# Kernel tuning notes

Measured on AMD Instinct MI355X. Metric: run time of the kernel, lower is better.

The kernel has to match this reference:

```python
import jax, jax.numpy as jnp
import numpy as np

NB, NSITES, N_NGB, DIM, NG = 32, 65536, 13, 3, 48


def setup_inputs() -> dict:
    key = jax.random.key(0)
    k1, k2, k3, k4, k5 = jax.random.split(key, 5)
    In = jax.random.normal(k1, (NB, 1, NSITES), dtype=jnp.float32)
    # wtVC ~ Normal(mean=1.0, std=0.1), size (dim, N_ngb)
    wtVC = 1.0 + 0.1 * jax.random.normal(k2, (DIM, N_NGB), dtype=jnp.float32)
    # gdiags: (Ng*dim, Ng*dim) symmetry-rotation mixing matrix
    gdiags = jax.random.normal(k3, (NG * DIM, NG * DIM), dtype=jnp.float32)
    GnnPerms = jax.random.randint(k4, (NG, N_NGB), 0, N_NGB)
    NNsites = jax.random.randint(k5, (N_NGB, NSITES), 0, NSITES)
    return {"In": In, "wtVC": wtVC, "gdiags": gdiags,
            "GnnPerms": GnnPerms, "NNsites": NNsites}


def reference(In, wtVC, gdiags, GnnPerms, NNsites):
    Ng = GnnPerms.shape[0]
    dim, n_ngb = wtVC.shape
    # RotateParams: row g*dim+d of the permuted weight is wtVC[d, GnnPerms[g]]
    Wp = wtVC[:, GnnPerms]                              # [dim, Ng, N_ngb]
    Wp = jnp.transpose(Wp, (1, 0, 2)).reshape(Ng * dim, n_ngb)
    Wt = gdiags @ Wp                                    # [Ng*dim, N_ngb]
    # Final op in torch is sum over g / Ng; fold that into the weight to
    # avoid materializing the [Nb, Ng*dim, Nsites] intermediate.
    Wmean = Wt.reshape(Ng, dim, n_ngb).mean(axis=0)     # [dim, N_ngb]
    # RearrangeInput: gathered[b, j, s] = In[b, 0, NNsites[j, s]]
    gathered = In[:, 0, :][:, NNsites]                  # [Nb, N_ngb, Nsites]
    # out[b, d, s] = sum_j Wmean[d, j] * gathered[b, j, s]
    return jnp.einsum('dj,bjs->bds', Wmean, gathered)   # [Nb, dim, Nsites]
```

## Files before the change

### kernel.cpp

```cpp
#include <hip/hip_runtime.h>

#define NB_     32
#define NSITES_ 65536
#define NNGB_   13
#define DIM_    3
#define NG_     48
#define GD_     (NG_ * DIM_)

typedef unsigned uvec4_t __attribute__((ext_vector_type(4)));

__global__ __launch_bounds__(256) void prep_kernel_78486(
    const float* __restrict__ In,
    const float* __restrict__ wtVC,
    const float* __restrict__ gdiags,
    const int*   __restrict__ perms,
    float*  __restrict__ wm,
    ushort* __restrict__ InT,
    int nTransBlocks)
{
    const int t = threadIdx.x;
    if ((int)blockIdx.x < DIM_ * NNGB_) {
        const int p = blockIdx.x;
        const int d = p / NNGB_, j = p - NNGB_ * d;
        __shared__ float wpj[GD_];
        __shared__ float red[4];
        if (t < GD_) {
            int g = t / DIM_, dp = t - DIM_ * g;
            wpj[t] = wtVC[dp * NNGB_ + perms[g * NNGB_ + j]];
        }
        __syncthreads();
        float acc = 0.f;
        for (int e = t; e < NG_ * GD_; e += 256) {
            int g = e / GD_;
            int k = e - g * GD_;
            acc += gdiags[(g * DIM_ + d) * GD_ + k] * wpj[k];
        }
#pragma unroll
        for (int off = 32; off > 0; off >>= 1) acc += __shfl_down(acc, off, 64);
        if ((t & 63) == 0) red[t >> 6] = acc;
        __syncthreads();
        if (t == 0) wm[p] = (red[0] + red[1] + red[2] + red[3]) * (1.0f / NG_);
    } else {
        const int tb = blockIdx.x - DIM_ * NNGB_;
        if (tb >= nTransBlocks) return;
        const int s0 = tb * 64;
        __shared__ ushort tile[64][40];
        const int sl = t & 63, bq = t >> 6;
#pragma unroll
        for (int r = 0; r < 8; r++) {
            int b = bq * 8 + r;
            float v = In[b * NSITES_ + s0 + sl];
            unsigned fu = __float_as_uint(v);
            fu = fu + 0x7FFFu + ((fu >> 16) & 1u);
            tile[sl][b] = (ushort)(fu >> 16);
        }
        __syncthreads();
        const int site = t >> 2, q = t & 3;
        uvec4_t val = *(const uvec4_t*)&tile[site][q * 8];
        *(uvec4_t*)(InT + (size_t)(s0 + site) * NB_ + q * 8) = val;
    }
}

__global__ __launch_bounds__(256) void gather_kernel_78486(
    const ushort* __restrict__ InT,
    const int*    __restrict__ nn,
    const float*  __restrict__ wm,
    float* __restrict__ out)
{
    const int t = blockIdx.x * 256 + threadIdx.x;
    const int q = t & 3;
    const int s = t >> 2;

    int idx[NNGB_];
#pragma unroll
    for (int j = 0; j < NNGB_; j++) idx[j] = nn[j * NSITES_ + s];

    uvec4_t u[NNGB_];
#pragma unroll
    for (int j = 0; j < NNGB_; j++)
        u[j] = *(const uvec4_t*)(InT + ((size_t)idx[j] << 5) + (q << 3));

    float a0[8], a1[8], a2[8];
#pragma unroll
    for (int i = 0; i < 8; i++) { a0[i] = 0.f; a1[i] = 0.f; a2[i] = 0.f; }

#pragma unroll
    for (int j = 0; j < NNGB_; j++) {
        unsigned uu[4] = {u[j].x, u[j].y, u[j].z, u[j].w};
        float v[8];
#pragma unroll
        for (int k = 0; k < 4; k++) {
            v[2 * k]     = __uint_as_float(uu[k] << 16);
            v[2 * k + 1] = __uint_as_float(uu[k] & 0xFFFF0000u);
        }
        float w0 = wm[j], w1 = wm[NNGB_ + j], w2 = wm[2 * NNGB_ + j];
#pragma unroll
        for (int i = 0; i < 8; i++) {
            a0[i] += w0 * v[i];
            a1[i] += w1 * v[i];
            a2[i] += w2 * v[i];
        }
    }

#pragma unroll
    for (int i = 0; i < 8; i++) {
        int b = q * 8 + i;
        size_t base = (size_t)b * DIM_ * NSITES_ + s;
        out[base]               = a0[i];
        out[base + NSITES_]     = a1[i];
        out[base + 2 * NSITES_] = a2[i];
    }
}

__global__ __launch_bounds__(256) void gather_fallback_78486(
    const float* __restrict__ In,
    const int*   __restrict__ nn,
    const float* __restrict__ wm,
    float* __restrict__ out)
{
    const int t = blockIdx.x * 256 + threadIdx.x;
    const int s = t & (NSITES_ - 1);
    const int b = t >> 16;
    float x0 = 0.f, x1 = 0.f, x2 = 0.f;
#pragma unroll
    for (int j = 0; j < NNGB_; j++) {
        int idx = nn[j * NSITES_ + s];
        float v = In[b * NSITES_ + idx];
        x0 += wm[0 * NNGB_ + j] * v;
        x1 += wm[1 * NNGB_ + j] * v;
        x2 += wm[2 * NNGB_ + j] * v;
    }
    out[(b * DIM_ + 0) * NSITES_ + s] = x0;
    out[(b * DIM_ + 1) * NSITES_ + s] = x1;
    out[(b * DIM_ + 2) * NSITES_ + s] = x2;
}

extern "C" void kernel_launch(void* const* d_in, const int* in_sizes, int n_in,
                              void* d_out, int out_size, void* d_ws, size_t ws_size,
                              hipStream_t stream)
{
    const float* In     = (const float*)d_in[0];
    const float* wtVC   = (const float*)d_in[1];
    const float* gdiags = (const float*)d_in[2];
    const int*   perms  = (const int*)d_in[3];
    const int*   nn     = (const int*)d_in[4];
    float* out = (float*)d_out;

    float*  wm  = (float*)d_ws;
    ushort* InT = (ushort*)((char*)d_ws + 1024);

    const size_t need = 1024 + (size_t)NSITES_ * NB_ * sizeof(ushort);
    const int nTrans = NSITES_ / 64;

    if (ws_size >= need) {
        prep_kernel_78486<<<DIM_ * NNGB_ + nTrans, 256, 0, stream>>>(
            In, wtVC, gdiags, perms, wm, InT, nTrans);
        gather_kernel_78486<<<(NSITES_ * 4) / 256, 256, 0, stream>>>(
            InT, nn, wm, out);
    } else {
        prep_kernel_78486<<<DIM_ * NNGB_, 256, 0, stream>>>(
            In, wtVC, gdiags, perms, wm, (ushort*)nullptr, 0);
        gather_fallback_78486<<<(NSITES_ * NB_) / 256, 256, 0, stream>>>(
            In, nn, wm, out);
    }
}
```

Baseline: 93.66 us.

## Fuse prep and gather kernels using a software grid barrier

Merges the weight-prep/transpose kernel and the gather kernel into one persistent-style launch of 1024 blocks. Each block transposes its tile and, for the first 39 blocks, computes the mean weights, then all blocks wait on a global atomic counter before doing the gather. This removes one kernel launch and the gap between kernels, but adds a memset launch and a spin barrier. The barrier relies on all 1024 blocks being co-resident (launch bounds request 4 blocks per SIMD-group), and it would deadlock if they are not.

```diff
diff --git a/kernel.cpp b/kernel.cpp
--- a/kernel.cpp
+++ b/kernel.cpp
@@ -9,23 +9,46 @@
 
 typedef unsigned uvec4_t __attribute__((ext_vector_type(4)));
 
-__global__ __launch_bounds__(256) void prep_kernel_78486(
+__global__ __launch_bounds__(256, 4) void fused_kernel_78486(
     const float* __restrict__ In,
     const float* __restrict__ wtVC,
     const float* __restrict__ gdiags,
     const int*   __restrict__ perms,
-    float*  __restrict__ wm,
-    ushort* __restrict__ InT,
-    int nTransBlocks)
-{
-    const int t = threadIdx.x;
-    if ((int)blockIdx.x < DIM_ * NNGB_) {
-        const int p = blockIdx.x;
+    const int*   __restrict__ nn,
+    float*    __restrict__ wm,
+    ushort*   __restrict__ InT,
+    unsigned* __restrict__ ctr,
+    float*    __restrict__ out)
+{
+    const int t   = threadIdx.x;
+    const int blk = blockIdx.x;
+
+    {
+        const int s0 = blk * 64;
+        __shared__ ushort tile[64][40];
+        const int sl = t & 63, bq = t >> 6;
+#pragma unroll
+        for (int r = 0; r < 8; r++) {
+            int b = bq * 8 + r;
+            float v = In[b * NSITES_ + s0 + sl];
+            unsigned fu = __float_as_uint(v);
+            fu = fu + 0x7FFFu + ((fu >> 16) & 1u);
+            tile[sl][b] = (ushort)(fu >> 16);
+        }
+        __syncthreads();
+        const int site = t >> 2, qq = t & 3;
+        uvec4_t val = *(const uvec4_t*)&tile[site][qq * 8];
+        *(uvec4_t*)(InT + (size_t)(s0 + site) * NB_ + qq * 8) = val;
+    }
+
+    if (blk < DIM_ * NNGB_) {
+        const int p = blk;
         const int d = p / NNGB_, j = p - NNGB_ * d;
         __shared__ float wpj[GD_];
         __shared__ float red[4];
         if (t < GD_) {
-            int g = t / DIM_, dp = t - DIM_ * g;
+            int g = t / DIM_;
+            int dp = t - DIM_ * g;
             wpj[t] = wtVC[dp * NNGB_ + perms[g * NNGB_ + j]];
         }
         __syncthreads();
@@ -40,36 +63,22 @@
         if ((t & 63) == 0) red[t >> 6] = acc;
         __syncthreads();
         if (t == 0) wm[p] = (red[0] + red[1] + red[2] + red[3]) * (1.0f / NG_);
-    } else {
-        const int tb = blockIdx.x - DIM_ * NNGB_;
-        if (tb >= nTransBlocks) return;
-        const int s0 = tb * 64;
-        __shared__ ushort tile[64][40];
-        const int sl = t & 63, bq = t >> 6;
-#pragma unroll
-        for (int r = 0; r < 8; r++) {
-            int b = bq * 8 + r;
-            float v = In[b * NSITES_ + s0 + sl];
-            unsigned fu = __float_as_uint(v);
-            fu = fu + 0x7FFFu + ((fu >> 16) & 1u);
-            tile[sl][b] = (ushort)(fu >> 16);
-        }
-        __syncthreads();
-        const int site = t >> 2, q = t & 3;
-        uvec4_t val = *(const uvec4_t*)&tile[site][q * 8];
-        *(uvec4_t*)(InT + (size_t)(s0 + site) * NB_ + q * 8) = val;
-    }
-}
-
-__global__ __launch_bounds__(256) void gather_kernel_78486(
-    const ushort* __restrict__ InT,
-    const int*    __restrict__ nn,
-    const float*  __restrict__ wm,
-    float* __restrict__ out)
-{
-    const int t = blockIdx.x * 256 + threadIdx.x;
-    const int q = t & 3;
-    const int s = t >> 2;
+    }
+
+    __syncthreads();
+    if (t == 0) {
+        __threadfence();
+        atomicAdd(ctr, 1u);
+        while (__hip_atomic_load(ctr, __ATOMIC_RELAXED,
+                                 __HIP_MEMORY_SCOPE_AGENT) < 1024u)
+            __builtin_amdgcn_s_sleep(8);
+        __threadfence();
+    }
+    __syncthreads();
+
+    const int gt = blk * 256 + t;
+    const int q  = gt & 3;
+    const int s  = gt >> 2;
 
     int idx[NNGB_];
 #pragma unroll
@@ -112,6 +121,35 @@
     }
 }
 
+__global__ __launch_bounds__(256) void prep_kernel_78486(
+    const float* __restrict__ wtVC,
+    const float* __restrict__ gdiags,
+    const int*   __restrict__ perms,
+    float*  __restrict__ wm)
+{
+    const int t = threadIdx.x;
+    const int p = blockIdx.x;
+    const int d = p / NNGB_, j = p - NNGB_ * d;
+    __shared__ float wpj[GD_];
+    __shared__ float red[4];
+    if (t < GD_) {
+        int g = t / DIM_, dp = t - DIM_ * g;
+        wpj[t] = wtVC[dp * NNGB_ + perms[g * NNGB_ + j]];
+    }
+    __syncthreads();
+    float acc = 0.f;
+    for (int e = t; e < NG_ * GD_; e += 256) {
+        int g = e / GD_;
+        int k = e - g * GD_;
+        acc += gdiags[(g * DIM_ + d) * GD_ + k] * wpj[k];
+    }
+#pragma unroll
+    for (int off = 32; off > 0; off >>= 1) acc += __shfl_down(acc, off, 64);
+    if ((t & 63) == 0) red[t >> 6] = acc;
+    __syncthreads();
+    if (t == 0) wm[p] = (red[0] + red[1] + red[2] + red[3]) * (1.0f / NG_);
+}
+
 __global__ __launch_bounds__(256) void gather_fallback_78486(
     const float* __restrict__ In,
     const int*   __restrict__ nn,
@@ -146,20 +184,19 @@
     const int*   nn     = (const int*)d_in[4];
     float* out = (float*)d_out;
 
-    float*  wm  = (float*)d_ws;
-    ushort* InT = (ushort*)((char*)d_ws + 1024);
+    float*    wm  = (float*)d_ws;
+    unsigned* ctr = (unsigned*)((char*)d_ws + 256);
+    ushort*   InT = (ushort*)((char*)d_ws + 1024);
 
     const size_t need = 1024 + (size_t)NSITES_ * NB_ * sizeof(ushort);
-    const int nTrans = NSITES_ / 64;
 
     if (ws_size >= need) {
-        prep_kernel_78486<<<DIM_ * NNGB_ + nTrans, 256, 0, stream>>>(
-            In, wtVC, gdiags, perms, wm, InT, nTrans);
-        gather_kernel_78486<<<(NSITES_ * 4) / 256, 256, 0, stream>>>(
-            InT, nn, wm, out);
+        hipMemsetAsync(ctr, 0, sizeof(unsigned), stream);
+        fused_kernel_78486<<<NSITES_ / 64, 256, 0, stream>>>(
+            In, wtVC, gdiags, perms, nn, wm, InT, ctr, out);
     } else {
         prep_kernel_78486<<<DIM_ * NNGB_, 256, 0, stream>>>(
-            In, wtVC, gdiags, perms, wm, (ushort*)nullptr, 0);
+            wtVC, gdiags, perms, wm);
         gather_fallback_78486<<<(NSITES_ * NB_) / 256, 256, 0, stream>>>(
             In, nn, wm, out);
     }
```

Measured after the change: 190.3 us. 103% more time.
